# Kernel tuning notes

Measured on AMD Instinct MI355X. Metric: run time of the kernel, lower is better.

## Reference

```python
import jax, jax.numpy as jnp
import numpy as np

T, H, I, E = 1024, 2048, 3200, 8  # tokens, hidden, intermediate, experts
JITTER_EPS = 0.01


def sparsemixer(scores, jitter_eps=JITTER_EPS):
    # ---- top-1 ----
    max1 = jnp.max(scores, axis=-1, keepdims=True)
    ind1 = jnp.argmax(scores, axis=-1, keepdims=True)  # first-max, matches torch
    factor = jnp.maximum(jnp.abs(scores), max1)        # clamp(min=max1)
    mask = (max1 - scores) / factor > 2.0 * jitter_eps
    masked_gates = jax.nn.softmax(jnp.where(mask, -jnp.inf, scores), axis=-1)
    mult1 = jnp.take_along_axis(masked_gates, ind1, axis=-1)
    # ---- mask out top-1, then top-2 ----
    top1_onehot = jax.nn.one_hot(ind1[..., 0], scores.shape[-1], dtype=bool)
    masked_scores = jnp.where(top1_onehot, -jnp.inf, scores)
    max2 = jnp.max(masked_scores, axis=-1, keepdims=True)
    ind2 = jnp.argmax(masked_scores, axis=-1, keepdims=True)
    factor2 = jnp.maximum(jnp.abs(scores), max2)
    mask2 = (max2 - scores) / factor2 > 2.0 * jitter_eps
    masked_gates2 = jax.nn.softmax(jnp.where(mask2, -jnp.inf, masked_scores), axis=-1)
    mult2 = jnp.take_along_axis(masked_gates2, ind2, axis=-1)
    multiplier = jnp.concatenate([mult1, mult2], axis=-1)       # [T, 2]
    selected = jnp.concatenate([ind1, ind2], axis=-1)           # [T, 2] int
    return multiplier, selected


def setup_inputs() -> dict:
    key = jax.random.key(0)
    k0, k1, k2, k3, k4 = jax.random.split(key, 5)
    hidden_states = jax.random.normal(k0, (T, H), dtype=jnp.float32)
    gate_w = jax.random.normal(k1, (E, H), dtype=jnp.float32) * (H ** -0.5)
    w1 = jax.random.normal(k2, (E, I, H), dtype=jnp.float32) * (H ** -0.5)
    w3 = jax.random.normal(k3, (E, I, H), dtype=jnp.float32) * (H ** -0.5)
    w2 = jax.random.normal(k4, (E, H, I), dtype=jnp.float32) * (I ** -0.5)
    return {"hidden_states": hidden_states, "gate_w": gate_w,
            "w1": w1, "w3": w3, "w2": w2}


def reference(hidden_states, gate_w, w1, w3, w2):
    x = hidden_states.reshape(-1, gate_w.shape[1])              # [T, H]
    router_logits = x @ gate_w.T                                # [T, E]
    topk_w, topk_ids = sparsemixer(router_logits)               # [T,2], [T,2]
    n_exp = gate_w.shape[0]
    # combine top-2 (weight, id) pairs into a dense [T, E] gate matrix
    gates = jnp.sum(jax.nn.one_hot(topk_ids, n_exp, dtype=x.dtype)
                    * topk_w[..., None], axis=1)                # [T, E]
    # SiLU-gated expert MLPs, combined with routing gates
    h1 = jnp.einsum('th,eih->tei', x, w1)                       # [T, E, I]
    h3 = jnp.einsum('th,eih->tei', x, w3)
    act = jax.nn.silu(h1) * h3                                  # [T, E, I]
    out = jnp.einsum('tei,ehi,te->th', act, w2, gates)          # [T, H]
    return out.reshape(hidden_states.shape)
```

## Files before the change

### kernel.cpp

```cpp
#include <hip/hip_runtime.h>

#define T_ 1024
#define H_ 2048
#define I_ 3200
#define E_ 8

typedef float fvec4 __attribute__((ext_vector_type(4)));
typedef float f32x4 __attribute__((ext_vector_type(4)));
typedef __bf16 bf16x8 __attribute__((ext_vector_type(8)));
typedef unsigned short u16x4 __attribute__((ext_vector_type(4)));

typedef const __attribute__((address_space(1))) void* gp1_t;
typedef __attribute__((address_space(3))) void* sp3_t;

#define WS_TOK   128
#define WS_GATE  32896
#define WS_XB    65664
#define WS_ACT   4259968

#define BARX() { asm volatile("s_waitcnt lgkmcnt(0)" ::: "memory"); \
    __builtin_amdgcn_sched_barrier(0); __builtin_amdgcn_s_barrier(); }

__global__ __launch_bounds__(256) void router_kernel(const float* __restrict__ x,
                                                     const float* __restrict__ gw,
                                                     int* __restrict__ cnt,
                                                     int* __restrict__ tok,
                                                     float* __restrict__ gate,
                                                     unsigned short* __restrict__ xb) {
  const int lane = threadIdx.x & 63;
  const int wv = threadIdx.x >> 6;
  const int t = blockIdx.x * 4 + wv;

  const float* xp = x + (size_t)t * H_;
  fvec4 xr[8];
#pragma unroll
  for (int j = 0; j < 8; ++j) xr[j] = *(const fvec4*)(xp + j * 256 + lane * 4);

  unsigned short* xbp = xb + (size_t)t * H_;
#pragma unroll
  for (int j = 0; j < 8; ++j) {
    u16x4 o;
#pragma unroll
    for (int c = 0; c < 4; ++c) o[c] = __builtin_bit_cast(unsigned short, (__bf16)xr[j][c]);
    *(u16x4*)(xbp + j * 256 + lane * 4) = o;
  }

  float s[E_];
#pragma unroll
  for (int e = 0; e < E_; ++e) {
    const float* gp = gw + (size_t)e * H_;
    float p = 0.f;
#pragma unroll
    for (int j = 0; j < 8; ++j) {
      fvec4 g = *(const fvec4*)(gp + j * 256 + lane * 4);
      p = fmaf(xr[j][0], g[0], p); p = fmaf(xr[j][1], g[1], p);
      p = fmaf(xr[j][2], g[2], p); p = fmaf(xr[j][3], g[3], p);
    }
#pragma unroll
    for (int off = 32; off > 0; off >>= 1) p += __shfl_xor(p, off);
    s[e] = p;
  }

  float max1 = s[0]; int i1 = 0;
#pragma unroll
  for (int e = 1; e < E_; ++e) if (s[e] > max1) { max1 = s[e]; i1 = e; }
  float den1 = 0.f;
#pragma unroll
  for (int e = 0; e < E_; ++e) {
    float factor = fmaxf(fabsf(s[e]), max1);
    if ((max1 - s[e]) <= 0.02f * factor) den1 += expf(s[e] - max1);
  }
  float mult1 = 1.f / den1;

  float max2 = -INFINITY; int i2 = 0;
#pragma unroll
  for (int e = 0; e < E_; ++e) if (e != i1 && s[e] > max2) { max2 = s[e]; i2 = e; }
  float den2 = 0.f;
#pragma unroll
  for (int e = 0; e < E_; ++e) {
    if (e == i1) continue;
    float factor = fmaxf(fabsf(s[e]), max2);
    if ((max2 - s[e]) <= 0.02f * factor) den2 += expf(s[e] - max2);
  }
  float mult2 = 1.f / den2;

  if (lane == 0) {
    int p1 = atomicAdd(&cnt[i1], 1); tok[i1 * T_ + p1] = t; gate[i1 * T_ + p1] = mult1;
    int p2 = atomicAdd(&cnt[i2], 1); tok[i2 * T_ + p2] = t; gate[i2 * T_ + p2] = mult2;
  }
}

__global__ void prefix_kernel(const int* __restrict__ cnt, int* __restrict__ base) {
  if (threadIdx.x == 0 && blockIdx.x == 0) {
    int a = 0;
    for (int e = 0; e < E_; ++e) { base[e] = a; a += (cnt[e] + 127) & ~127; }
    base[E_] = a;
  }
}

__global__ __launch_bounds__(512, 2) void ffn1_kernel(
    const unsigned short* __restrict__ xb, const float* __restrict__ w1,
    const float* __restrict__ w3, const int* __restrict__ cnt,
    const int* __restrict__ base, const int* __restrict__ tokl,
    unsigned short* __restrict__ actb) {
  const int e = blockIdx.z;
  const int ab = base[e];
  const int padcnt = base[e + 1] - ab;
  const int m_base = blockIdx.y * 256;
  if (m_base >= padcnt) return;
  const int count = cnt[e];
  const int n0 = blockIdx.x * 64;
  const int tid = threadIdx.x;
  const int lane = tid & 63, wv = tid >> 6;
  const int wm = wv >> 1, wn = wv & 1;

  __shared__ unsigned short Ash[3][256 * 64];
  __shared__ unsigned short B1s[2][64 * 64];
  __shared__ unsigned short B3s[2][64 * 64];

  const unsigned short* aSrc[4];
  const int colg = ((lane & 7) ^ ((lane >> 3) & 7)) * 8;
#pragma unroll
  for (int i = 0; i < 4; ++i) {
    int r = m_base + wv * 32 + i * 8 + (lane >> 3);
    if (r >= count) r = count - 1;
    aSrc[i] = xb + (size_t)tokl[e * T_ + r] * H_ + colg;
  }
  const int brow = tid >> 3;
  const float* b1p = w1 + ((size_t)e * I_ + n0 + brow) * H_ + (tid & 7) * 8;
  const float* b3p = w3 + ((size_t)e * I_ + n0 + brow) * H_ + (tid & 7) * 8;
  const int wbyte = brow * 128 + (((tid & 7) ^ (brow & 7)) << 4);

  int rb[2][2];
#pragma unroll
  for (int ni = 0; ni < 2; ++ni) {
    int br_ = wn * 32 + ni * 16 + (lane & 15);
#pragma unroll
    for (int kk = 0; kk < 2; ++kk)
      rb[ni][kk] = br_ * 128 + (((kk * 4 + (lane >> 4)) ^ (br_ & 7)) << 4);
  }

  f32x4 acc1[4][2], acc3[4][2];
#pragma unroll
  for (int mi = 0; mi < 4; ++mi)
#pragma unroll
    for (int ni = 0; ni < 2; ++ni) { acc1[mi][ni] = (f32x4){0,0,0,0}; acc3[mi][ni] = (f32x4){0,0,0,0}; }

  auto STAGE_A = [&](unsigned short* dst, int kb) {
#pragma unroll
    for (int i = 0; i < 4; ++i)
      __builtin_amdgcn_global_load_lds((gp1_t)(aSrc[i] + kb),
                                       (sp3_t)(dst + (wv * 32 + i * 8) * 64), 16, 0, 0);
  };
  auto LOADB = [&](fvec4 (&r1)[2], fvec4 (&r3)[2], int kb) {
    r1[0] = *(const fvec4*)(b1p + kb); r1[1] = *(const fvec4*)(b1p + kb + 4);
    r3[0] = *(const fvec4*)(b3p + kb); r3[1] = *(const fvec4*)(b3p + kb + 4);
  };
  auto CVTW = [&](fvec4 (&r1)[2], fvec4 (&r3)[2], int buf) {
    bf16x8 v, w;
#pragma unroll
    for (int c = 0; c < 4; ++c) {
      v[c] = (__bf16)r1[0][c]; v[c + 4] = (__bf16)r1[1][c];
      w[c] = (__bf16)r3[0][c]; w[c + 4] = (__bf16)r3[1][c];
    }
    *(bf16x8*)((char*)B1s[buf] + wbyte) = v;
    *(bf16x8*)((char*)B3s[buf] + wbyte) = w;
  };
  auto FRAGA = [&](bf16x8 (&af)[4][2], const unsigned short* Ab) {
#pragma unroll
    for (int mi = 0; mi < 4; ++mi) {
      int ar = wm * 64 + mi * 16 + (lane & 15);
#pragma unroll
      for (int kk = 0; kk < 2; ++kk)
        af[mi][kk] = *(const bf16x8*)((const char*)Ab + ar * 128 +
                                      (((kk * 4 + (lane >> 4)) ^ (ar & 7)) << 4));
    }
  };
  auto COMPUTE = [&](bf16x8 (&af)[4][2], int buf) {
    __builtin_amdgcn_s_setprio(1);
#pragma unroll
    for (int kk = 0; kk < 2; ++kk) {
      bf16x8 f1[2], f3[2];
#pragma unroll
      for (int ni = 0; ni < 2; ++ni) {
        f1[ni] = *(const bf16x8*)((const char*)B1s[buf] + rb[ni][kk]);
        f3[ni] = *(const bf16x8*)((const char*)B3s[buf] + rb[ni][kk]);
      }
#pragma unroll
      for (int mi = 0; mi < 4; ++mi)
#pragma unroll
        for (int ni = 0; ni < 2; ++ni) {
          acc1[mi][ni] = __builtin_amdgcn_mfma_f32_16x16x32_bf16(af[mi][kk], f1[ni], acc1[mi][ni], 0, 0, 0);
          acc3[mi][ni] = __builtin_amdgcn_mfma_f32_16x16x32_bf16(af[mi][kk], f3[ni], acc3[mi][ni], 0, 0, 0);
        }
    }
    __builtin_amdgcn_s_setprio(0);
  };

  const int NT = H_ / 64;
  unsigned short *A0 = Ash[0], *A1 = Ash[1], *A2 = Ash[2];
  fvec4 b1e[2], b3e[2], b1o[2], b3o[2];
  bf16x8 af[4][2];

  STAGE_A(A0, 0);
  LOADB(b1e, b3e, 0);
  STAGE_A(A1, 64);
  LOADB(b1o, b3o, 64);
  asm volatile("s_waitcnt vmcnt(8)" ::: "memory");
  CVTW(b1e, b3e, 0);
  BARX();

  for (int t = 0; t < NT; t += 2) {
    if (t + 2 < NT) { STAGE_A(A2, (t + 2) * 64); LOADB(b1e, b3e, (t + 2) * 64); }
    FRAGA(af, A0);
    COMPUTE(af, 0);
    if (t + 2 < NT) { asm volatile("s_waitcnt vmcnt(8)" ::: "memory"); }
    else            { asm volatile("s_waitcnt vmcnt(0)" ::: "memory"); }
    CVTW(b1o, b3o, 1);
    BARX();
    if (t + 3 < NT) { STAGE_A(A0, (t + 3) * 64); LOADB(b1o, b3o, (t + 3) * 64); }
    FRAGA(af, A1);
    COMPUTE(af, 1);
    if (t + 2 < NT) {
      if (t + 3 < NT) { asm volatile("s_waitcnt vmcnt(8)" ::: "memory"); }
      else            { asm volatile("s_waitcnt vmcnt(0)" ::: "memory"); }
      CVTW(b1e, b3e, 0);
    }
    BARX();
    unsigned short* tmp = A2; A2 = A1; A1 = A0; A0 = tmp;
  }

  const int row_lim = padcnt - m_base;
#pragma unroll
  for (int mi = 0; mi < 4; ++mi)
#pragma unroll
    for (int ni = 0; ni < 2; ++ni)
#pragma unroll
      for (int j = 0; j < 4; ++j) {
        int row = wm * 64 + mi * 16 + (lane >> 4) * 4 + j;
        if (row < row_lim) {
          float h1 = acc1[mi][ni][j];
          float a = (h1 / (1.f + __expf(-h1))) * acc3[mi][ni][j];
          actb[(size_t)(ab + m_base + row) * I_ + n0 + wn * 32 + ni * 16 + (lane & 15)] =
              __builtin_bit_cast(unsigned short, (__bf16)a);
        }
      }
}

__global__ __launch_bounds__(512, 2) void ffn2_kernel(
    const unsigned short* __restrict__ actb, const float* __restrict__ w2,
    const int* __restrict__ cnt, const int* __restrict__ base,
    const int* __restrict__ tokl, const float* __restrict__ gatel,
    float* __restrict__ out) {
  const int e = blockIdx.z;
  const int count = cnt[e];
  const int m_base = blockIdx.y * 256;
  if (m_base >= count) return;
  const int ab = base[e];
  const int n0 = blockIdx.x * 64;
  const int tid = threadIdx.x;
  const int lane = tid & 63, wv = tid >> 6;
  const int wm = wv >> 1, wn = wv & 1;

  __shared__ unsigned short Ash[3][256 * 64];
  __shared__ unsigned short Bs[2][64 * 64];

  const unsigned short* aSrc[4];
  const int colg = ((lane & 7) ^ ((lane >> 3) & 7)) * 8;
#pragma unroll
  for (int i = 0; i < 4; ++i) {
    int r = ab + m_base + wv * 32 + i * 8 + (lane >> 3);
    aSrc[i] = actb + (size_t)r * I_ + colg;
  }
  const int brow = tid >> 3;
  const float* bp = w2 + ((size_t)e * H_ + n0 + brow) * I_ + (tid & 7) * 8;
  const int wbyte = brow * 128 + (((tid & 7) ^ (brow & 7)) << 4);

  int rb[2][2];
#pragma unroll
  for (int ni = 0; ni < 2; ++ni) {
    int br_ = wn * 32 + ni * 16 + (lane & 15);
#pragma unroll
    for (int kk = 0; kk < 2; ++kk)
      rb[ni][kk] = br_ * 128 + (((kk * 4 + (lane >> 4)) ^ (br_ & 7)) << 4);
  }

  f32x4 acc[4][2];
#pragma unroll
  for (int mi = 0; mi < 4; ++mi)
#pragma unroll
    for (int ni = 0; ni < 2; ++ni) acc[mi][ni] = (f32x4){0,0,0,0};

  auto STAGE_A = [&](unsigned short* dst, int kb) {
#pragma unroll
    for (int i = 0; i < 4; ++i)
      __builtin_amdgcn_global_load_lds((gp1_t)(aSrc[i] + kb),
                                       (sp3_t)(dst + (wv * 32 + i * 8) * 64), 16, 0, 0);
  };
  auto LOADB = [&](fvec4 (&r)[2], int kb) {
    r[0] = *(const fvec4*)(bp + kb); r[1] = *(const fvec4*)(bp + kb + 4);
  };
  auto CVTW = [&](fvec4 (&r)[2], int buf) {
    bf16x8 v;
#pragma unroll
    for (int c = 0; c < 4; ++c) { v[c] = (__bf16)r[0][c]; v[c + 4] = (__bf16)r[1][c]; }
    *(bf16x8*)((char*)Bs[buf] + wbyte) = v;
  };
  auto FRAGA = [&](bf16x8 (&af)[4][2], const unsigned short* Ab) {
#pragma unroll
    for (int mi = 0; mi < 4; ++mi) {
      int ar = wm * 64 + mi * 16 + (lane & 15);
#pragma unroll
      for (int kk = 0; kk < 2; ++kk)
        af[mi][kk] = *(const bf16x8*)((const char*)Ab + ar * 128 +
                                      (((kk * 4 + (lane >> 4)) ^ (ar & 7)) << 4));
    }
  };
  auto COMPUTE = [&](bf16x8 (&af)[4][2], int buf) {
    __builtin_amdgcn_s_setprio(1);
#pragma unroll
    for (int kk = 0; kk < 2; ++kk) {
      bf16x8 f[2];
#pragma unroll
      for (int ni = 0; ni < 2; ++ni)
        f[ni] = *(const bf16x8*)((const char*)Bs[buf] + rb[ni][kk]);
#pragma unroll
      for (int mi = 0; mi < 4; ++mi)
#pragma unroll
        for (int ni = 0; ni < 2; ++ni)
          acc[mi][ni] = __builtin_amdgcn_mfma_f32_16x16x32_bf16(af[mi][kk], f[ni], acc[mi][ni], 0, 0, 0);
    }
    __builtin_amdgcn_s_setprio(0);
  };

  const int NT = I_ / 64;
  unsigned short *A0 = Ash[0], *A1 = Ash[1], *A2 = Ash[2];
  fvec4 be[2], bo[2];
  bf16x8 af[4][2];

  STAGE_A(A0, 0);
  LOADB(be, 0);
  STAGE_A(A1, 64);
  LOADB(bo, 64);
  asm volatile("s_waitcnt vmcnt(6)" ::: "memory");
  CVTW(be, 0);
  BARX();

  for (int t = 0; t < NT; t += 2) {
    if (t + 2 < NT) { STAGE_A(A2, (t + 2) * 64); LOADB(be, (t + 2) * 64); }
    FRAGA(af, A0);
    COMPUTE(af, 0);
    if (t + 2 < NT) { asm volatile("s_waitcnt vmcnt(6)" ::: "memory"); }
    else            { asm volatile("s_waitcnt vmcnt(0)" ::: "memory"); }
    CVTW(bo, 1);
    BARX();
    if (t + 3 < NT) { STAGE_A(A0, (t + 3) * 64); LOADB(bo, (t + 3) * 64); }
    FRAGA(af, A1);
    COMPUTE(af, 1);
    if (t + 2 < NT) {
      if (t + 3 < NT) { asm volatile("s_waitcnt vmcnt(6)" ::: "memory"); }
      else            { asm volatile("s_waitcnt vmcnt(0)" ::: "memory"); }
      CVTW(be, 0);
    }
    BARX();
    unsigned short* tmp = A2; A2 = A1; A1 = A0; A0 = tmp;
  }

#pragma unroll
  for (int mi = 0; mi < 4; ++mi)
#pragma unroll
    for (int j = 0; j < 4; ++j) {
      int row = m_base + wm * 64 + mi * 16 + (lane >> 4) * 4 + j;
      if (row < count) {
        int tokv = tokl[e * T_ + row];
        float g = gatel[e * T_ + row];
#pragma unroll
        for (int ni = 0; ni < 2; ++ni)
          atomicAdd(&out[(size_t)tokv * H_ + n0 + wn * 32 + ni * 16 + (lane & 15)],
                    g * acc[mi][ni][j]);
      }
    }
}

extern "C" void kernel_launch(void* const* d_in, const int* in_sizes, int n_in,
                              void* d_out, int out_size, void* d_ws, size_t ws_size,
                              hipStream_t stream) {
  const float* x  = (const float*)d_in[0];
  const float* gw = (const float*)d_in[1];
  const float* w1 = (const float*)d_in[2];
  const float* w3 = (const float*)d_in[3];
  const float* w2 = (const float*)d_in[4];
  float* out = (float*)d_out;
  char* ws = (char*)d_ws;

  int* cnt = (int*)ws;
  int* base = (int*)(ws + 64);
  int* tokl = (int*)(ws + WS_TOK);
  float* gatel = (float*)(ws + WS_GATE);
  unsigned short* xb = (unsigned short*)(ws + WS_XB);
  unsigned short* actb = (unsigned short*)(ws + WS_ACT);

  (void)hipMemsetAsync(d_out, 0, (size_t)T_ * H_ * sizeof(float), stream);
  (void)hipMemsetAsync(ws, 0, 64, stream);

  router_kernel<<<T_ / 4, 256, 0, stream>>>(x, gw, cnt, tokl, gatel, xb);
  prefix_kernel<<<1, 64, 0, stream>>>(cnt, base);
  ffn1_kernel<<<dim3(I_ / 64, 4, E_), 512, 0, stream>>>(xb, w1, w3, cnt, base, tokl, actb);
  ffn2_kernel<<<dim3(H_ / 64, 4, E_), 512, 0, stream>>>(actb, w2, cnt, base, tokl, gatel, out);
}
```

Measured before the change: 352.7 us.

## Schedule FFN blocks over compacted per-expert 128-row chunks with 256-thread blocks

After: 393.0 us. 11.4% more time.

```diff
diff --git a/kernel.cpp b/kernel.cpp
--- a/kernel.cpp
+++ b/kernel.cpp
@@ -13,10 +13,12 @@
 typedef const __attribute__((address_space(1))) void* gp1_t;
 typedef __attribute__((address_space(3))) void* sp3_t;
 
-#define WS_TOK   128
-#define WS_GATE  32896
-#define WS_XB    65664
-#define WS_ACT   4259968
+#define WS_CHUNK 128
+#define WS_TOK   512
+#define WS_GATE  33280
+#define WS_XB    66560
+#define WS_ACT   4261888
+#define MAXCH    24
 
 #define BARX() { asm volatile("s_waitcnt lgkmcnt(0)" ::: "memory"); \
     __builtin_amdgcn_sched_barrier(0); __builtin_amdgcn_s_barrier(); }
@@ -90,31 +92,37 @@
   }
 }
 
-__global__ void prefix_kernel(const int* __restrict__ cnt, int* __restrict__ base) {
+__global__ void prefix_kernel(const int* __restrict__ cnt, int* __restrict__ base,
+                              int* __restrict__ chunk) {
   if (threadIdx.x == 0 && blockIdx.x == 0) {
-    int a = 0;
-    for (int e = 0; e < E_; ++e) { base[e] = a; a += (cnt[e] + 127) & ~127; }
+    int a = 0, c = 0;
+    for (int e = 0; e < E_; ++e) {
+      base[e] = a;
+      int pc = (cnt[e] + 127) & ~127;
+      for (int m = 0; m < pc; m += 128) { chunk[1 + c] = e; chunk[1 + MAXCH + c] = m; ++c; }
+      a += pc;
+    }
     base[E_] = a;
+    chunk[0] = c;
   }
 }
 
-__global__ __launch_bounds__(512, 2) void ffn1_kernel(
+__global__ __launch_bounds__(256) void ffn1_kernel(
     const unsigned short* __restrict__ xb, const float* __restrict__ w1,
     const float* __restrict__ w3, const int* __restrict__ cnt,
-    const int* __restrict__ base, const int* __restrict__ tokl,
-    unsigned short* __restrict__ actb) {
-  const int e = blockIdx.z;
+    const int* __restrict__ base, const int* __restrict__ chunk,
+    const int* __restrict__ tokl, unsigned short* __restrict__ actb) {
+  if ((int)blockIdx.y >= chunk[0]) return;
+  const int e = chunk[1 + blockIdx.y];
+  const int m_base = chunk[1 + MAXCH + blockIdx.y];
   const int ab = base[e];
-  const int padcnt = base[e + 1] - ab;
-  const int m_base = blockIdx.y * 256;
-  if (m_base >= padcnt) return;
   const int count = cnt[e];
   const int n0 = blockIdx.x * 64;
   const int tid = threadIdx.x;
   const int lane = tid & 63, wv = tid >> 6;
   const int wm = wv >> 1, wn = wv & 1;
 
-  __shared__ unsigned short Ash[3][256 * 64];
+  __shared__ unsigned short Ash[3][128 * 64];
   __shared__ unsigned short B1s[2][64 * 64];
   __shared__ unsigned short B3s[2][64 * 64];
 
@@ -126,10 +134,13 @@
     if (r >= count) r = count - 1;
     aSrc[i] = xb + (size_t)tokl[e * T_ + r] * H_ + colg;
   }
-  const int brow = tid >> 3;
-  const float* b1p = w1 + ((size_t)e * I_ + n0 + brow) * H_ + (tid & 7) * 8;
-  const float* b3p = w3 + ((size_t)e * I_ + n0 + brow) * H_ + (tid & 7) * 8;
-  const int wbyte = brow * 128 + (((tid & 7) ^ (brow & 7)) << 4);
+  const int brow = tid >> 2;
+  const int bc = (tid & 3) * 16;
+  const float* b1p = w1 + ((size_t)e * I_ + n0 + brow) * H_ + bc;
+  const float* b3p = w3 + ((size_t)e * I_ + n0 + brow) * H_ + bc;
+  const int c0 = (tid & 3) * 2;
+  const int wb0 = brow * 128 + (((c0 + 0) ^ (brow & 7)) << 4);
+  const int wb1 = brow * 128 + (((c0 + 1) ^ (brow & 7)) << 4);
 
   int rb[2][2];
 #pragma unroll
@@ -152,19 +163,26 @@
       __builtin_amdgcn_global_load_lds((gp1_t)(aSrc[i] + kb),
                                        (sp3_t)(dst + (wv * 32 + i * 8) * 64), 16, 0, 0);
   };
-  auto LOADB = [&](fvec4 (&r1)[2], fvec4 (&r3)[2], int kb) {
-    r1[0] = *(const fvec4*)(b1p + kb); r1[1] = *(const fvec4*)(b1p + kb + 4);
-    r3[0] = *(const fvec4*)(b3p + kb); r3[1] = *(const fvec4*)(b3p + kb + 4);
-  };
-  auto CVTW = [&](fvec4 (&r1)[2], fvec4 (&r3)[2], int buf) {
-    bf16x8 v, w;
+  auto LOADB = [&](fvec4 (&r1)[4], fvec4 (&r3)[4], int kb) {
+#pragma unroll
+    for (int j = 0; j < 4; ++j) {
+      r1[j] = *(const fvec4*)(b1p + kb + j * 4);
+      r3[j] = *(const fvec4*)(b3p + kb + j * 4);
+    }
+  };
+  auto CVTW = [&](fvec4 (&r1)[4], fvec4 (&r3)[4], int buf) {
+    bf16x8 v0, v1, w0, w1v;
 #pragma unroll
     for (int c = 0; c < 4; ++c) {
-      v[c] = (__bf16)r1[0][c]; v[c + 4] = (__bf16)r1[1][c];
-      w[c] = (__bf16)r3[0][c]; w[c + 4] = (__bf16)r3[1][c];
-    }
-    *(bf16x8*)((char*)B1s[buf] + wbyte) = v;
-    *(bf16x8*)((char*)B3s[buf] + wbyte) = w;
+      v0[c] = (__bf16)r1[0][c]; v0[c + 4] = (__bf16)r1[1][c];
+      v1[c] = (__bf16)r1[2][c]; v1[c + 4] = (__bf16)r1[3][c];
+      w0[c] = (__bf16)r3[0][c]; w0[c + 4] = (__bf16)r3[1][c];
+      w1v[c] = (__bf16)r3[2][c]; w1v[c + 4] = (__bf16)r3[3][c];
+    }
+    *(bf16x8*)((char*)B1s[buf] + wb0) = v0;
+    *(bf16x8*)((char*)B1s[buf] + wb1) = v1;
+    *(bf16x8*)((char*)B3s[buf] + wb0) = w0;
+    *(bf16x8*)((char*)B3s[buf] + wb1) = w1v;
   };
   auto FRAGA = [&](bf16x8 (&af)[4][2], const unsigned short* Ab) {
 #pragma unroll
@@ -199,14 +217,14 @@
 
   const int NT = H_ / 64;
   unsigned short *A0 = Ash[0], *A1 = Ash[1], *A2 = Ash[2];
-  fvec4 b1e[2], b3e[2], b1o[2], b3o[2];
+  fvec4 b1e[4], b3e[4], b1o[4], b3o[4];
   bf16x8 af[4][2];
 
   STAGE_A(A0, 0);
   LOADB(b1e, b3e, 0);
   STAGE_A(A1, 64);
   LOADB(b1o, b3o, 64);
-  asm volatile("s_waitcnt vmcnt(8)" ::: "memory");
+  asm volatile("s_waitcnt vmcnt(12)" ::: "memory");
   CVTW(b1e, b3e, 0);
   BARX();
 
@@ -214,7 +232,7 @@
     if (t + 2 < NT) { STAGE_A(A2, (t + 2) * 64); LOADB(b1e, b3e, (t + 2) * 64); }
     FRAGA(af, A0);
     COMPUTE(af, 0);
-    if (t + 2 < NT) { asm volatile("s_waitcnt vmcnt(8)" ::: "memory"); }
+    if (t + 2 < NT) { asm volatile("s_waitcnt vmcnt(12)" ::: "memory"); }
     else            { asm volatile("s_waitcnt vmcnt(0)" ::: "memory"); }
     CVTW(b1o, b3o, 1);
     BARX();
@@ -222,7 +240,7 @@
     FRAGA(af, A1);
     COMPUTE(af, 1);
     if (t + 2 < NT) {
-      if (t + 3 < NT) { asm volatile("s_waitcnt vmcnt(8)" ::: "memory"); }
+      if (t + 3 < NT) { asm volatile("s_waitcnt vmcnt(12)" ::: "memory"); }
       else            { asm volatile("s_waitcnt vmcnt(0)" ::: "memory"); }
       CVTW(b1e, b3e, 0);
     }
@@ -230,6 +248,7 @@
     unsigned short* tmp = A2; A2 = A1; A1 = A0; A0 = tmp;
   }
 
+  const int padcnt = base[e + 1] - ab;
   const int row_lim = padcnt - m_base;
 #pragma unroll
   for (int mi = 0; mi < 4; ++mi)
@@ -247,22 +266,25 @@
       }
 }
 
-__global__ __launch_bounds__(512, 2) void ffn2_kernel(
+__global__ __launch_bounds__(256) void ffn2_kernel(
     const unsigned short* __restrict__ actb, const float* __restrict__ w2,
     const int* __restrict__ cnt, const int* __restrict__ base,
-    const int* __restrict__ tokl, const float* __restrict__ gatel,
-    float* __restrict__ out) {
-  const int e = blockIdx.z;
+    const int* __restrict__ chunk, const int* __restrict__ tokl,
+    const float* __restrict__ gatel, float* __restrict__ out) {
+  if ((int)blockIdx.y >= chunk[0]) return;
+  const int e = chunk[1 + blockIdx.y];
+  const int m_base = chunk[1 + MAXCH + blockIdx.y];
   const int count = cnt[e];
-  const int m_base = blockIdx.y * 256;
-  if (m_base >= count) return;
+  if (m_base >= count) {
+    return;
+  }
   const int ab = base[e];
   const int n0 = blockIdx.x * 64;
   const int tid = threadIdx.x;
   const int lane = tid & 63, wv = tid >> 6;
   const int wm = wv >> 1, wn = wv & 1;
 
-  __shared__ unsigned short Ash[3][256 * 64];
+  __shared__ unsigned short Ash[3][128 * 64];
   __shared__ unsigned short Bs[2][64 * 64];
 
   const unsigned short* aSrc[4];
@@ -272,9 +294,12 @@
     int r = ab + m_base + wv * 32 + i * 8 + (lane >> 3);
     aSrc[i] = actb + (size_t)r * I_ + colg;
   }
-  const int brow = tid >> 3;
-  const float* bp = w2 + ((size_t)e * H_ + n0 + brow) * I_ + (tid & 7) * 8;
-  const int wbyte = brow * 128 + (((tid & 7) ^ (brow & 7)) << 4);
+  const int brow = tid >> 2;
+  const int bc = (tid & 3) * 16;
+  const float* bp = w2 + ((size_t)e * H_ + n0 + brow) * I_ + bc;
+  const int c0 = (tid & 3) * 2;
+  const int wb0 = brow * 128 + (((c0 + 0) ^ (brow & 7)) << 4);
+  const int wb1 = brow * 128 + (((c0 + 1) ^ (brow & 7)) << 4);
 
   int rb[2][2];
 #pragma unroll
@@ -297,14 +322,19 @@
       __builtin_amdgcn_global_load_lds((gp1_t)(aSrc[i] + kb),
                                        (sp3_t)(dst + (wv * 32 + i * 8) * 64), 16, 0, 0);
   };
-  auto LOADB = [&](fvec4 (&r)[2], int kb) {
-    r[0] = *(const fvec4*)(bp + kb); r[1] = *(const fvec4*)(bp + kb + 4);
-  };
-  auto CVTW = [&](fvec4 (&r)[2], int buf) {
-    bf16x8 v;
-#pragma unroll
-    for (int c = 0; c < 4; ++c) { v[c] = (__bf16)r[0][c]; v[c + 4] = (__bf16)r[1][c]; }
-    *(bf16x8*)((char*)Bs[buf] + wbyte) = v;
+  auto LOADB = [&](fvec4 (&r)[4], int kb) {
+#pragma unroll
+    for (int j = 0; j < 4; ++j) r[j] = *(const fvec4*)(bp + kb + j * 4);
+  };
+  auto CVTW = [&](fvec4 (&r)[4], int buf) {
+    bf16x8 v0, v1;
+#pragma unroll
+    for (int c = 0; c < 4; ++c) {
+      v0[c] = (__bf16)r[0][c]; v0[c + 4] = (__bf16)r[1][c];
+      v1[c] = (__bf16)r[2][c]; v1[c + 4] = (__bf16)r[3][c];
+    }
+    *(bf16x8*)((char*)Bs[buf] + wb0) = v0;
+    *(bf16x8*)((char*)Bs[buf] + wb1) = v1;
   };
   auto FRAGA = [&](bf16x8 (&af)[4][2], const unsigned short* Ab) {
 #pragma unroll
@@ -335,14 +365,14 @@
 
   const int NT = I_ / 64;
   unsigned short *A0 = Ash[0], *A1 = Ash[1], *A2 = Ash[2];
-  fvec4 be[2], bo[2];
+  fvec4 be[4], bo[4];
   bf16x8 af[4][2];
 
   STAGE_A(A0, 0);
   LOADB(be, 0);
   STAGE_A(A1, 64);
   LOADB(bo, 64);
-  asm volatile("s_waitcnt vmcnt(6)" ::: "memory");
+  asm volatile("s_waitcnt vmcnt(8)" ::: "memory");
   CVTW(be, 0);
   BARX();
 
@@ -350,7 +380,7 @@
     if (t + 2 < NT) { STAGE_A(A2, (t + 2) * 64); LOADB(be, (t + 2) * 64); }
     FRAGA(af, A0);
     COMPUTE(af, 0);
-    if (t + 2 < NT) { asm volatile("s_waitcnt vmcnt(6)" ::: "memory"); }
+    if (t + 2 < NT) { asm volatile("s_waitcnt vmcnt(8)" ::: "memory"); }
     else            { asm volatile("s_waitcnt vmcnt(0)" ::: "memory"); }
     CVTW(bo, 1);
     BARX();
@@ -358,7 +388,7 @@
     FRAGA(af, A1);
     COMPUTE(af, 1);
     if (t + 2 < NT) {
-      if (t + 3 < NT) { asm volatile("s_waitcnt vmcnt(6)" ::: "memory"); }
+      if (t + 3 < NT) { asm volatile("s_waitcnt vmcnt(8)" ::: "memory"); }
       else            { asm volatile("s_waitcnt vmcnt(0)" ::: "memory"); }
       CVTW(be, 0);
     }
@@ -395,6 +425,7 @@
 
   int* cnt = (int*)ws;
   int* base = (int*)(ws + 64);
+  int* chunk = (int*)(ws + WS_CHUNK);
   int* tokl = (int*)(ws + WS_TOK);
   float* gatel = (float*)(ws + WS_GATE);
   unsigned short* xb = (unsigned short*)(ws + WS_XB);
@@ -404,7 +435,7 @@
   (void)hipMemsetAsync(ws, 0, 64, stream);
 
   router_kernel<<<T_ / 4, 256, 0, stream>>>(x, gw, cnt, tokl, gatel, xb);
-  prefix_kernel<<<1, 64, 0, stream>>>(cnt, base);
-  ffn1_kernel<<<dim3(I_ / 64, 4, E_), 512, 0, stream>>>(xb, w1, w3, cnt, base, tokl, actb);
-  ffn2_kernel<<<dim3(H_ / 64, 4, E_), 512, 0, stream>>>(actb, w2, cnt, base, tokl, gatel, out);
+  prefix_kernel<<<1, 64, 0, stream>>>(cnt, base, chunk);
+  ffn1_kernel<<<dim3(I_ / 64, MAXCH), 256, 0, stream>>>(xb, w1, w3, cnt, base, chunk, tokl, actb);
+  ffn2_kernel<<<dim3(H_ / 64, MAXCH), 256, 0, stream>>>(actb, w2, cnt, base, chunk, tokl, gatel, out);
 }
```
